# Kernel tuning notes

Hardware: AMD Instinct MI355X
Metric: run time of the kernel (lower is better)

Reference implementation:

```python
import jax, jax.numpy as jnp
import numpy as np

N = 100000
E = 1600000
IN_DIM = 256
OUT_DIM = 128
LEAKY_SLOPE = 0.01  # torch nn.LeakyReLU default


def setup_inputs() -> dict:
    key = jax.random.key(0)
    k1, k2, k3, k4, k5 = jax.random.split(key, 5)
    features = jax.random.normal(k1, (N, IN_DIM), dtype=jnp.float32)
    # xavier_uniform for weight [out, in]
    limit = float(np.sqrt(6.0 / (IN_DIM + OUT_DIM)))
    weight = jax.random.uniform(k2, (OUT_DIM, IN_DIM), dtype=jnp.float32,
                                minval=-limit, maxval=limit)
    edge_rows = jnp.sort(jax.random.randint(k3, (E,), 0, N, dtype=jnp.int32))
    edge_cols = jax.random.randint(k4, (E,), 0, N, dtype=jnp.int32)
    edge_vals = jax.random.uniform(k5, (E,), dtype=jnp.float32)
    return {"features": features, "weight": weight,
            "edge_rows": edge_rows, "edge_cols": edge_cols,
            "edge_vals": edge_vals}


def reference(features, weight, edge_rows, edge_cols, edge_vals):
    # support = LeakyReLU(features @ W^T)   [N, OUT_DIM]
    support = jax.nn.leaky_relu(jnp.einsum('ni,oi->no', features, weight),
                                negative_slope=LEAKY_SLOPE)
    # SpMM: out[r] = sum over edges (r, c, v) of v * support[c]
    msgs = support[edge_cols] * edge_vals[:, None]  # [E, OUT_DIM]
    out = jax.ops.segment_sum(msgs, edge_rows, num_segments=N)
    return out
```

## Files before the change

kernel.cpp:

```cpp
#include <hip/hip_runtime.h>

#define IN_DIM 256
#define OUT_DIM 128
#define LEAKY 0.01f
#define GEMM_BLOCKS 512

typedef __attribute__((ext_vector_type(8))) short bf16x8;
typedef __attribute__((ext_vector_type(4))) float f32x4;
typedef __attribute__((ext_vector_type(4))) unsigned u32x4;

__device__ inline unsigned cvtpk_bf16(float lo, float hi) {
  unsigned r;
  asm volatile("v_cvt_pk_bf16_f32 %0, %1, %2" : "=v"(r) : "v"(lo), "v"(hi));
  return r;
}

__device__ inline float blo(unsigned u) {
  union { unsigned x; float f; } c; c.x = u << 16; return c.f;
}
__device__ inline float bhi(unsigned u) {
  union { unsigned x; float f; } c; c.x = u & 0xFFFF0000u; return c.f;
}

__device__ inline int swz_byte(int r, int u) {
  return r * 512 + ((u & 16) << 4) + (((u & 15) ^ (r & 15)) << 4);
}

__global__ __launch_bounds__(512, 4) void gemm_scan(
    const float* __restrict__ feat, const float* __restrict__ w,
    const int* __restrict__ erows, unsigned short* __restrict__ support,
    int* __restrict__ rs, int nrows, int nedges, int ntiles) {
  if (blockIdx.x >= GEMM_BLOCKS) {
    const int i = (blockIdx.x - GEMM_BLOCKS) * 512 + threadIdx.x;
    if (i >= nedges) return;
    const int cur  = erows[i];
    const int prev = (i == 0) ? -1 : erows[i - 1];
    for (int r = prev + 1; r <= cur; ++r) rs[r] = i;
    if (i == nedges - 1)
      for (int r = cur + 1; r <= nrows; ++r) rs[r] = nedges;
    return;
  }

  __shared__ alignas(16) unsigned short wlds[128 * 256];
  char* wb = reinterpret_cast<char*>(wlds);

  const int t = threadIdx.x;
#pragma unroll
  for (int it = 0; it < 8; ++it) {
    const int g = it * 512 + t;
    const int r = g >> 5;
    const int u = g & 31;
    const float* src = w + r * IN_DIM + u * 8;
    const float4 a = *reinterpret_cast<const float4*>(src);
    const float4 b = *reinterpret_cast<const float4*>(src + 4);
    uint4 pk;
    pk.x = cvtpk_bf16(a.x, a.y);
    pk.y = cvtpk_bf16(a.z, a.w);
    pk.z = cvtpk_bf16(b.x, b.y);
    pk.w = cvtpk_bf16(b.z, b.w);
    *reinterpret_cast<uint4*>(wb + swz_byte(r, u)) = pk;
  }
  __syncthreads();

  const int wid  = t >> 6;
  const int lane = t & 63;
  const int lrow = lane & 15;
  const int hi   = lane >> 4;

  for (int tile = blockIdx.x; tile < ntiles; tile += GEMM_BLOCKS) {
    const int mrow = tile * 128 + wid * 16 + lrow;
    const int mr   = mrow < nrows ? mrow : nrows - 1;
    const float* fp = feat + mr * IN_DIM + hi * 8;

    f32x4 acc[8];
#pragma unroll
    for (int nt = 0; nt < 8; ++nt) acc[nt] = (f32x4){0.f, 0.f, 0.f, 0.f};

#pragma unroll
    for (int ks = 0; ks < 8; ++ks) {
      const float4 a = *reinterpret_cast<const float4*>(fp + ks * 32);
      const float4 b = *reinterpret_cast<const float4*>(fp + ks * 32 + 4);
      union { bf16x8 v; unsigned u[4]; } bf;
      bf.u[0] = cvtpk_bf16(a.x, a.y);
      bf.u[1] = cvtpk_bf16(a.z, a.w);
      bf.u[2] = cvtpk_bf16(b.x, b.y);
      bf.u[3] = cvtpk_bf16(b.z, b.w);
      const int u = ks * 4 + hi;
#pragma unroll
      for (int nt = 0; nt < 8; ++nt) {
        const bf16x8 af = *reinterpret_cast<const bf16x8*>(
            wb + swz_byte(nt * 16 + lrow, u));
        acc[nt] = __builtin_amdgcn_mfma_f32_16x16x32_bf16(af, bf.v, acc[nt],
                                                          0, 0, 0);
      }
    }

    if (mrow < nrows) {
      unsigned short* orow = support + mrow * OUT_DIM + hi * 4;
#pragma unroll
      for (int nt = 0; nt < 8; ++nt) {
        f32x4 v = acc[nt];
        float a0 = v[0] > 0.f ? v[0] : LEAKY * v[0];
        float a1 = v[1] > 0.f ? v[1] : LEAKY * v[1];
        float a2 = v[2] > 0.f ? v[2] : LEAKY * v[2];
        float a3 = v[3] > 0.f ? v[3] : LEAKY * v[3];
        uint2 st;
        st.x = cvtpk_bf16(a0, a1);
        st.y = cvtpk_bf16(a2, a3);
        *reinterpret_cast<uint2*>(orow + nt * 16) = st;
      }
    }
  }
}

__global__ __launch_bounds__(256) void spmm_bf16(
    const int* __restrict__ rs, const int* __restrict__ ecols,
    const float* __restrict__ evals, const unsigned short* __restrict__ support,
    float* __restrict__ out, int nrows) {
  const int t    = threadIdx.x;
  const int lane = t & 15;
  const int row  = blockIdx.x * 16 + (t >> 4);
  if (row >= nrows) return;

  const int s = rs[row];
  const int e = rs[row + 1];

  f32x4 accA[4], accB[4];
#pragma unroll
  for (int j = 0; j < 4; ++j) {
    accA[j] = (f32x4){0.f, 0.f, 0.f, 0.f};
    accB[j] = (f32x4){0.f, 0.f, 0.f, 0.f};
  }

  const unsigned short* srow = support + lane * 8;

  for (int i = s; i < e; i += 8) {
    int   ii[8];
    float vv[8];
#pragma unroll
    for (int j = 0; j < 8; ++j) {
      const int  idx = i + j;
      const bool ok  = idx < e;
      ii[j] = ok ? idx : e - 1;
      vv[j] = ok ? evals[ii[j]] : 0.f;
    }
#pragma unroll
    for (int j = 0; j < 8; ++j) {
      const int c = ecols[ii[j]];
      const u32x4 u =
          *reinterpret_cast<const u32x4*>(srow + (size_t)c * OUT_DIM);
      const int   k = j & 3;
      const float v = vv[j];
      accA[k][0] += v * blo(u[0]);
      accA[k][1] += v * bhi(u[0]);
      accA[k][2] += v * blo(u[1]);
      accA[k][3] += v * bhi(u[1]);
      accB[k][0] += v * blo(u[2]);
      accB[k][1] += v * bhi(u[2]);
      accB[k][2] += v * blo(u[3]);
      accB[k][3] += v * bhi(u[3]);
    }
  }

#pragma unroll
  for (int j = 1; j < 4; ++j) {
    accA[0] += accA[j];
    accB[0] += accB[j];
  }
  float* orow = out + (size_t)row * OUT_DIM + lane * 8;
  __builtin_nontemporal_store(accA[0], reinterpret_cast<f32x4*>(orow));
  __builtin_nontemporal_store(accB[0], reinterpret_cast<f32x4*>(orow + 4));
}

extern "C" void kernel_launch(void* const* d_in, const int* in_sizes, int n_in,
                              void* d_out, int out_size, void* d_ws,
                              size_t ws_size, hipStream_t stream) {
  const float* features = (const float*)d_in[0];
  const float* weight   = (const float*)d_in[1];
  const int*   erows    = (const int*)d_in[2];
  const int*   ecols    = (const int*)d_in[3];
  const float* evals    = (const float*)d_in[4];
  float*       out      = (float*)d_out;

  const int nrows  = in_sizes[0] / IN_DIM;
  const int nedges = in_sizes[2];

  unsigned short* support = (unsigned short*)d_ws;
  int* rs = (int*)((char*)d_ws + (size_t)nrows * OUT_DIM * 2);

  const int ntiles      = (nrows + 127) / 128;
  const int scan_blocks = (nedges + 511) / 512;

  gemm_scan<<<GEMM_BLOCKS + scan_blocks, 512, 0, stream>>>(
      features, weight, erows, support, rs, nrows, nedges, ntiles);
  spmm_bf16<<<(nrows + 15) / 16, 256, 0, stream>>>(rs, ecols, evals, support,
                                                   out, nrows);
}
```

Measured before the change: 94.46 us.

## Store support in column slices and stage edge lists in LDS for SpMM

The GEMM now writes the bf16 support matrix as eight column slices of 16 columns each, instead of row-major. The SpMM kernel assigns two threads per row and walks the slices one after another, so each pass gathers from a 3.2 MB slice that may stay cache-resident. Each block first stages its edge (col,val) pairs into LDS. Every row's edge list is now re-read eight times, and the parallelism per row drops from 16 lanes to 2, which can lengthen the per-thread serial loop on long rows and weakens memory coalescing.

```diff
diff --git a/kernel.cpp b/kernel.cpp
--- a/kernel.cpp
+++ b/kernel.cpp
@@ -3,7 +3,10 @@
 #define IN_DIM 256
 #define OUT_DIM 128
 #define LEAKY 0.01f
-#define GEMM_BLOCKS 512
+#define GEMM_BLOCKS 391
+#define NSLICE 8
+#define SP_ROWS 128
+#define SP_CAP 3072
 
 typedef __attribute__((ext_vector_type(8))) short bf16x8;
 typedef __attribute__((ext_vector_type(4))) float f32x4;
@@ -20,6 +23,9 @@
 }
 __device__ inline float bhi(unsigned u) {
   union { unsigned x; float f; } c; c.x = u & 0xFFFF0000u; return c.f;
+}
+__device__ inline float asf(unsigned u) {
+  union { unsigned x; float f; } c; c.x = u; return c.f;
 }
 
 __device__ inline int swz_byte(int r, int u) {
@@ -66,6 +72,7 @@
   const int lane = t & 63;
   const int lrow = lane & 15;
   const int hi   = lane >> 4;
+  const size_t slice_stride = (size_t)nrows * 16;
 
   for (int tile = blockIdx.x; tile < ntiles; tile += GEMM_BLOCKS) {
     const int mrow = tile * 128 + wid * 16 + lrow;
@@ -96,7 +103,6 @@
     }
 
     if (mrow < nrows) {
-      unsigned short* orow = support + mrow * OUT_DIM + hi * 4;
 #pragma unroll
       for (int nt = 0; nt < 8; ++nt) {
         f32x4 v = acc[nt];
@@ -107,69 +113,80 @@
         uint2 st;
         st.x = cvtpk_bf16(a0, a1);
         st.y = cvtpk_bf16(a2, a3);
-        *reinterpret_cast<uint2*>(orow + nt * 16) = st;
+        unsigned short* o =
+            support + nt * slice_stride + (size_t)mrow * 16 + hi * 4;
+        *reinterpret_cast<uint2*>(o) = st;
       }
     }
   }
 }
 
-__global__ __launch_bounds__(256) void spmm_bf16(
+__global__ __launch_bounds__(256) void spmm_slice(
     const int* __restrict__ rs, const int* __restrict__ ecols,
     const float* __restrict__ evals, const unsigned short* __restrict__ support,
     float* __restrict__ out, int nrows) {
+  __shared__ uint2 lev[SP_CAP];
   const int t    = threadIdx.x;
-  const int lane = t & 15;
-  const int row  = blockIdx.x * 16 + (t >> 4);
+  const int r0   = blockIdx.x * SP_ROWS;
+  const int rend = (r0 + SP_ROWS < nrows) ? r0 + SP_ROWS : nrows;
+  const int cs   = rs[r0];
+  const int ce   = rs[rend];
+  const int cnt  = ce - cs;
+
+  const int lim = cnt < SP_CAP ? cnt : SP_CAP;
+  for (int k = t; k < lim; k += 256)
+    lev[k] = make_uint2((unsigned)ecols[cs + k], __float_as_uint(evals[cs + k]));
+  __syncthreads();
+
+  const int row = r0 + (t >> 1);
+  const int h   = t & 1;
   if (row >= nrows) return;
 
-  const int s = rs[row];
-  const int e = rs[row + 1];
-
-  f32x4 accA[4], accB[4];
-#pragma unroll
-  for (int j = 0; j < 4; ++j) {
-    accA[j] = (f32x4){0.f, 0.f, 0.f, 0.f};
-    accB[j] = (f32x4){0.f, 0.f, 0.f, 0.f};
-  }
-
-  const unsigned short* srow = support + lane * 8;
-
-  for (int i = s; i < e; i += 8) {
-    int   ii[8];
-    float vv[8];
-#pragma unroll
-    for (int j = 0; j < 8; ++j) {
-      const int  idx = i + j;
-      const bool ok  = idx < e;
-      ii[j] = ok ? idx : e - 1;
-      vv[j] = ok ? evals[ii[j]] : 0.f;
+  const int s_ = rs[row] - cs;
+  const int e_ = rs[row + 1] - cs;
+
+  for (int s = 0; s < NSLICE; ++s) {
+    const unsigned short* sbase = support + (size_t)s * nrows * 16 + h * 8;
+    f32x4 aA = {0.f, 0.f, 0.f, 0.f}, aB = {0.f, 0.f, 0.f, 0.f};
+
+    for (int base = s_; base < e_; base += 8) {
+      unsigned cj[8];
+      float    vj[8];
+#pragma unroll
+      for (int j = 0; j < 8; ++j) {
+        int k = base + j;
+        const bool ok = k < e_;
+        k = ok ? k : e_ - 1;
+        uint2 p;
+        if (k < SP_CAP) {
+          p = lev[k];
+        } else {
+          p = make_uint2((unsigned)ecols[cs + k],
+                         __float_as_uint(evals[cs + k]));
+        }
+        cj[j] = p.x;
+        vj[j] = ok ? asf(p.y) : 0.f;
+      }
+#pragma unroll
+      for (int j = 0; j < 8; ++j) {
+        const u32x4 u =
+            *reinterpret_cast<const u32x4*>(sbase + (size_t)cj[j] * 16);
+        const float v = vj[j];
+        aA[0] += v * blo(u[0]);
+        aA[1] += v * bhi(u[0]);
+        aA[2] += v * blo(u[1]);
+        aA[3] += v * bhi(u[1]);
+        aB[0] += v * blo(u[2]);
+        aB[1] += v * bhi(u[2]);
+        aB[2] += v * blo(u[3]);
+        aB[3] += v * bhi(u[3]);
+      }
     }
-#pragma unroll
-    for (int j = 0; j < 8; ++j) {
-      const int c = ecols[ii[j]];
-      const u32x4 u =
-          *reinterpret_cast<const u32x4*>(srow + (size_t)c * OUT_DIM);
-      const int   k = j & 3;
-      const float v = vv[j];
-      accA[k][0] += v * blo(u[0]);
-      accA[k][1] += v * bhi(u[0]);
-      accA[k][2] += v * blo(u[1]);
-      accA[k][3] += v * bhi(u[1]);
-      accB[k][0] += v * blo(u[2]);
-      accB[k][1] += v * bhi(u[2]);
-      accB[k][2] += v * blo(u[3]);
-      accB[k][3] += v * bhi(u[3]);
-    }
-  }
-
-#pragma unroll
-  for (int j = 1; j < 4; ++j) {
-    accA[0] += accA[j];
-    accB[0] += accB[j];
-  }
-  float* orow = out + (size_t)row * OUT_DIM + lane * 8;
-  __builtin_nontemporal_store(accA[0], reinterpret_cast<f32x4*>(orow));
-  __builtin_nontemporal_store(accB[0], reinterpret_cast<f32x4*>(orow + 4));
+
+    float* o = out + (size_t)row * OUT_DIM + s * 16 + h * 8;
+    *reinterpret_cast<f32x4*>(o)     = aA;
+    *reinterpret_cast<f32x4*>(o + 4) = aB;
+  }
 }
 
 extern "C" void kernel_launch(void* const* d_in, const int* in_sizes, int n_in,
@@ -193,6 +210,6 @@
 
   gemm_scan<<<GEMM_BLOCKS + scan_blocks, 512, 0, stream>>>(
       features, weight, erows, support, rs, nrows, nedges, ntiles);
-  spmm_bf16<<<(nrows + 15) / 16, 256, 0, stream>>>(rs, ecols, evals, support,
-                                                   out, nrows);
-}
+  spmm_slice<<<(nrows + SP_ROWS - 1) / SP_ROWS, 256, 0, stream>>>(
+      rs, ecols, evals, support, out, nrows);
+}
```

Measured after the change: 192.4 us. 2.04x slower.
